# Kernel tuning notes

Measured on AMD Instinct MI355X. Metric: run time of the kernel, lower is better.

## Reference

```python
import jax, jax.numpy as jnp
import numpy as np


def _mlp(h, W1, b1, W2, b2):
    # Linear -> ReLU -> Linear
    h = jax.nn.relu(h @ W1 + b1)
    return h @ W2 + b2


def setup_inputs() -> dict:
    key = jax.random.key(0)
    ks = jax.random.split(key, 8)
    N, E, DN, DE, H, O = 50000, 800000, 128, 64, 256, 128
    DIN = DN + DE  # 192
    s1 = 1.0 / np.sqrt(DIN)
    s2 = 1.0 / np.sqrt(H)
    return {
        "x": jax.random.normal(ks[0], (N, DN), dtype=jnp.float32),
        "edge_index": jax.random.randint(ks[1], (2, E), 0, N, dtype=jnp.int32),
        "edge_attr": jax.random.normal(ks[2], (E, DE), dtype=jnp.float32),
        "W1_out": jax.random.normal(ks[3], (DIN, H), dtype=jnp.float32) * s1,
        "b1_out": jnp.zeros((H,), dtype=jnp.float32),
        "W2_out": jax.random.normal(ks[4], (H, O), dtype=jnp.float32) * s2,
        "b2_out": jnp.zeros((O,), dtype=jnp.float32),
        "W1_in": jax.random.normal(ks[5], (DIN, H), dtype=jnp.float32) * s1,
        "b1_in": jnp.zeros((H,), dtype=jnp.float32),
        "W2_in": jax.random.normal(ks[6], (H, O), dtype=jnp.float32) * s2,
        "b2_in": jnp.zeros((O,), dtype=jnp.float32),
    }


def reference(x, edge_index, edge_attr, W1_out, b1_out, W2_out, b2_out,
              W1_in, b1_in, W2_in, b2_in):
    N = x.shape[0]
    row, col = edge_index[0], edge_index[1]
    # Shared gather + concat: [E, d_node + d_edge]
    msg_in = jnp.concatenate([x[col], edge_attr], axis=1)

    # flow_out: edges with row < col. Compute MLP densely, zero masked edges,
    # then scatter-sum -> identical math to masked gather + scatter-sum.
    m_out = (row < col).astype(x.dtype)[:, None]
    flow_out = _mlp(msg_in, W1_out, b1_out, W2_out, b2_out) * m_out
    flow_out = jax.ops.segment_sum(flow_out, row, num_segments=N)

    # flow_in: edges with row > col
    m_in = (row > col).astype(x.dtype)[:, None]
    flow_in = _mlp(msg_in, W1_in, b1_in, W2_in, b2_in) * m_in
    flow_in = jax.ops.segment_sum(flow_in, row, num_segments=N)

    return jnp.concatenate((flow_in, flow_out), axis=1)  # [N, 2*O]
```

## Files before the change

kernel.cpp:

```cpp
#include <hip/hip_runtime.h>
#include <hip/hip_bf16.h>

typedef __attribute__((ext_vector_type(8))) short short8;
typedef __attribute__((ext_vector_type(8))) unsigned short ushort8;
typedef __attribute__((ext_vector_type(4))) float f32x4;

#define DN   128
#define DE   64
#define DIN  192
#define HID  256
#define OUTD 128
#define TE   128
#define NT   512
#define MSG_LD 200
#define H_LD   264
#define OUT_LD 132

static __device__ __forceinline__ unsigned short f2b(float f) {
    unsigned int u = __float_as_uint(f);
    u += 0x7fffu + ((u >> 16) & 1u);
    return (unsigned short)(u >> 16);
}

__global__ __launch_bounds__(256)
void prep_kernel(const float* __restrict__ W1o, const float* __restrict__ W1i,
                 const float* __restrict__ W2o, const float* __restrict__ W2i,
                 unsigned short* __restrict__ W1po, unsigned short* __restrict__ W1pi,
                 unsigned short* __restrict__ W2po, unsigned short* __restrict__ W2pi,
                 const int* __restrict__ ei, int E, int N, int* __restrict__ hist,
                 const float* __restrict__ x, unsigned short* __restrict__ xb) {
    const int S1 = DIN * HID, S2v = HID * OUTD;
    const int PACKN = 2 * S1 + 2 * S2v;
    int idx = blockIdx.x * blockDim.x + threadIdx.x;
    if (idx < PACKN) {
        const float* W; unsigned short* Wp; int Nc, j;
        if      (idx < S1)          { W = W1o; Wp = W1po; Nc = HID;  j = idx; }
        else if (idx < 2*S1)        { W = W1i; Wp = W1pi; Nc = HID;  j = idx - S1; }
        else if (idx < 2*S1 + S2v)  { W = W2o; Wp = W2po; Nc = OUTD; j = idx - 2*S1; }
        else                        { W = W2i; Wp = W2pi; Nc = OUTD; j = idx - 2*S1 - S2v; }
        int k = j / Nc, n = j - k * Nc;
        Wp[(((k >> 5) * Nc + n) << 5) + (k & 31)] = f2b(W[j]);
    } else if (idx < PACKN + E) {
        int e = idx - PACKN;
        int r = ei[e], c = ei[E + e];
        if      (r < c) atomicAdd(&hist[r], 1);
        else if (r > c) atomicAdd(&hist[N + r], 1);
    } else {
        int i = idx - PACKN - E;
        if (i < N * DN / 8) {
            float4 a = reinterpret_cast<const float4*>(x)[i * 2];
            float4 b = reinterpret_cast<const float4*>(x)[i * 2 + 1];
            ushort8 v = { f2b(a.x), f2b(a.y), f2b(a.z), f2b(a.w),
                          f2b(b.x), f2b(b.y), f2b(b.z), f2b(b.w) };
            reinterpret_cast<ushort8*>(xb)[i] = v;
        }
    }
}

__global__ __launch_bounds__(1024)
void scan1_kernel(const int* __restrict__ hist, int* __restrict__ cursor,
                  int* __restrict__ chunkSum, int N, int nch) {
    __shared__ int s_ws[16];
    const int br = blockIdx.x / nch, ch = blockIdx.x - br * nch;
    const int tid = threadIdx.x, lane = tid & 63, wv = tid >> 6;
    const int i = ch * 1024 + tid;
    int v = (i < N) ? hist[(size_t)br * N + i] : 0;
    int incl = v;
    #pragma unroll
    for (int d = 1; d < 64; d <<= 1) {
        int t = __shfl_up(incl, d, 64);
        if (lane >= d) incl += t;
    }
    if (lane == 63) s_ws[wv] = incl;
    __syncthreads();
    if (tid < 16) {
        int w = s_ws[tid];
        int wi = w;
        #pragma unroll
        for (int d = 1; d < 16; d <<= 1) {
            int t = __shfl_up(wi, d, 64);
            if (tid >= d) wi += t;
        }
        s_ws[tid] = wi - w;
    }
    __syncthreads();
    int excl = s_ws[wv] + incl - v;
    if (i < N) cursor[(size_t)br * N + i] = excl;
    if (tid == 1023) chunkSum[br * nch + ch] = excl + v;
}

__global__ __launch_bounds__(128)
void scan2_kernel(int* __restrict__ chunkSum, int* __restrict__ cnt, int nch) {
    const int br = threadIdx.x >> 6, lane = threadIdx.x & 63;
    int v = (lane < nch) ? chunkSum[br * nch + lane] : 0;
    int incl = v;
    #pragma unroll
    for (int d = 1; d < 64; d <<= 1) {
        int t = __shfl_up(incl, d, 64);
        if (lane >= d) incl += t;
    }
    if (lane < nch) chunkSum[br * nch + lane] = incl - v;
    if (lane == nch - 1) cnt[br] = incl;
}

__global__ __launch_bounds__(256)
void reorder_kernel(const int* __restrict__ ei, int E, int N, int nch,
                    int* __restrict__ cursor, const int* __restrict__ chunkSum,
                    int* __restrict__ list_out, int* __restrict__ list_in) {
    int e = blockIdx.x * blockDim.x + threadIdx.x;
    if (e >= E) return;
    int r = ei[e], c = ei[E + e];
    if (r == c) return;
    int br = (r < c) ? 0 : 1;
    int p = chunkSum[br * nch + (r >> 10)] + atomicAdd(&cursor[(size_t)br * N + r], 1);
    (br ? list_in : list_out)[p] = e;
}

__global__ __launch_bounds__(NT, 4)
void mlp_scatter_kernel(const unsigned short* __restrict__ xb,
                        const int* __restrict__ ei,
                        const float* __restrict__ ea,
                        const unsigned short* __restrict__ W1p_out,
                        const unsigned short* __restrict__ W1p_in,
                        const float* __restrict__ b1_out,
                        const float* __restrict__ b1_in,
                        const unsigned short* __restrict__ W2p_out,
                        const unsigned short* __restrict__ W2p_in,
                        const float* __restrict__ b2_out,
                        const float* __restrict__ b2_in,
                        const int* __restrict__ list_out,
                        const int* __restrict__ list_in,
                        const int* __restrict__ cnt,
                        float* __restrict__ out,
                        int E, int nbpb) {
    __shared__ __align__(16) unsigned short s_buf[TE * H_LD];
    __shared__ int s_eid[TE], s_dest[TE], s_col[TE];

    const int branch = (blockIdx.x >= nbpb) ? 1 : 0;
    const int lb = blockIdx.x - branch * nbpb;
    const int count = cnt[branch];
    if (lb * TE >= count) return;
    const int* list            = branch ? list_in : list_out;
    const unsigned short* W1p  = branch ? W1p_in  : W1p_out;
    const float* b1            = branch ? b1_in   : b1_out;
    const unsigned short* W2p  = branch ? W2p_in  : W2p_out;
    const float* b2            = branch ? b2_in   : b2_out;
    const int colbase          = branch ? 0 : OUTD;

    const int tid = threadIdx.x;
    if (tid < TE) {
        int idx = lb * TE + tid;
        int e = (idx < count) ? list[idx] : -1;
        s_eid[tid]  = e;
        s_dest[tid] = (e >= 0) ? ei[e] : -1;
        s_col[tid]  = (e >= 0) ? ei[E + e] : 0;
    }
    __syncthreads();

    {
        const int le  = tid >> 2;
        const int sub = tid & 3;
        const int e   = s_eid[le];
        const ushort8* xrow = reinterpret_cast<const ushort8*>(xb) + (size_t)s_col[le] * (DN / 8);
        #pragma unroll
        for (int j = 0; j < 4; ++j) {
            int seg = sub + j * 4;
            ushort8 v = {0, 0, 0, 0, 0, 0, 0, 0};
            if (e >= 0) v = xrow[seg];
            *reinterpret_cast<ushort8*>(&s_buf[le * MSG_LD + seg * 8]) = v;
        }
        const float4* erow = reinterpret_cast<const float4*>(ea) + (size_t)e * (DE / 4);
        #pragma unroll
        for (int j = 0; j < 4; ++j) {
            float4 v = make_float4(0.f, 0.f, 0.f, 0.f);
            if (e >= 0) v = erow[sub * 4 + j];
            unsigned int lo = (unsigned int)f2b(v.x) | ((unsigned int)f2b(v.y) << 16);
            unsigned int hi = (unsigned int)f2b(v.z) | ((unsigned int)f2b(v.w) << 16);
            *reinterpret_cast<uint2*>(&s_buf[le * MSG_LD + DN + sub * 16 + j * 4]) = make_uint2(lo, hi);
        }
    }
    __syncthreads();

    const int wave = tid >> 6;
    const int lane = tid & 63;
    const int ln   = lane & 15;
    const int quad = lane >> 4;

    f32x4 acc[8][2];
    {
        const int nbase = wave * 32;
        float bias[2];
        #pragma unroll
        for (int t = 0; t < 2; ++t) bias[t] = b1[nbase + t * 16 + ln];
        #pragma unroll
        for (int mt = 0; mt < 8; ++mt)
            #pragma unroll
            for (int t = 0; t < 2; ++t)
                acc[mt][t] = (f32x4){bias[t], bias[t], bias[t], bias[t]};
        #pragma unroll
        for (int kt = 0; kt < DIN / 32; ++kt) {
            short8 a[8], b[2];
            #pragma unroll
            for (int mt = 0; mt < 8; ++mt)
                a[mt] = *reinterpret_cast<const short8*>(
                    &s_buf[(mt * 16 + ln) * MSG_LD + kt * 32 + quad * 8]);
            #pragma unroll
            for (int t = 0; t < 2; ++t)
                b[t] = *reinterpret_cast<const short8*>(
                    &W1p[((kt * HID + nbase + t * 16 + ln) << 5) + quad * 8]);
            #pragma unroll
            for (int mt = 0; mt < 8; ++mt)
                #pragma unroll
                for (int t = 0; t < 2; ++t)
                    acc[mt][t] = __builtin_amdgcn_mfma_f32_16x16x32_bf16(a[mt], b[t], acc[mt][t], 0, 0, 0);
        }
    }
    __syncthreads();

    {
        const int nbase = wave * 32;
        #pragma unroll
        for (int mt = 0; mt < 8; ++mt)
            #pragma unroll
            for (int t = 0; t < 2; ++t) {
                int ncol = nbase + t * 16 + ln;
                #pragma unroll
                for (int r = 0; r < 4; ++r) {
                    int m = mt * 16 + quad * 4 + r;
                    float v = acc[mt][t][r];
                    s_buf[m * H_LD + ncol] = f2b(v > 0.f ? v : 0.f);
                }
            }
    }
    __syncthreads();

    f32x4 acc2[8];
    {
        const int nbase = wave * 16;
        float bias2 = b2[nbase + ln];
        #pragma unroll
        for (int mt = 0; mt < 8; ++mt)
            acc2[mt] = (f32x4){bias2, bias2, bias2, bias2};
        #pragma unroll
        for (int kt = 0; kt < HID / 32; ++kt) {
            short8 a[8], b;
            #pragma unroll
            for (int mt = 0; mt < 8; ++mt)
                a[mt] = *reinterpret_cast<const short8*>(
                    &s_buf[(mt * 16 + ln) * H_LD + kt * 32 + quad * 8]);
            b = *reinterpret_cast<const short8*>(
                &W2p[((kt * OUTD + nbase + ln) << 5) + quad * 8]);
            #pragma unroll
            for (int mt = 0; mt < 8; ++mt)
                acc2[mt] = __builtin_amdgcn_mfma_f32_16x16x32_bf16(a[mt], b, acc2[mt], 0, 0, 0);
        }
    }
    __syncthreads();

    float* s_outf = reinterpret_cast<float*>(s_buf);
    {
        const int nbase = wave * 16;
        #pragma unroll
        for (int mt = 0; mt < 8; ++mt)
            #pragma unroll
            for (int r = 0; r < 4; ++r)
                s_outf[(mt * 16 + quad * 4 + r) * OUT_LD + nbase + ln] = acc2[mt][r];
    }
    __syncthreads();

    {
        const int c  = tid & 127;
        const int m0 = (tid >> 7) * 32;
        float run = 0.f;
        int cur = -1, rs = m0;
        for (int m = m0; m < m0 + 32; ++m) {
            int d = s_dest[m];
            float v = s_outf[m * OUT_LD + c];
            if (d != cur) {
                if (cur >= 0) {
                    float* p = &out[(size_t)cur * (2 * OUTD) + colbase + c];
                    if (rs > m0) *p = run; else atomicAdd(p, run);
                }
                cur = d; run = 0.f; rs = m;
            }
            if (d >= 0) run += v;
        }
        if (cur >= 0)
            atomicAdd(&out[(size_t)cur * (2 * OUTD) + colbase + c], run);
    }
}

extern "C" void kernel_launch(void* const* d_in, const int* in_sizes, int n_in,
                              void* d_out, int out_size, void* d_ws, size_t ws_size,
                              hipStream_t stream) {
    const float* x   = (const float*)d_in[0];
    const int*   ei  = (const int*)d_in[1];
    const float* ea  = (const float*)d_in[2];
    const float* W1o = (const float*)d_in[3];
    const float* b1o = (const float*)d_in[4];
    const float* W2o = (const float*)d_in[5];
    const float* b2o = (const float*)d_in[6];
    const float* W1i = (const float*)d_in[7];
    const float* b1i = (const float*)d_in[8];
    const float* W2i = (const float*)d_in[9];
    const float* b2i = (const float*)d_in[10];
    float* out = (float*)d_out;
    const int E = in_sizes[1] / 2;
    const int N = in_sizes[0] / DN;
    const int nch = (N + 1023) >> 10;

    int* cnt      = (int*)d_ws;
    int* chunkSum = cnt + 16;
    int* hist     = chunkSum + 128;
    int* cursor   = hist + 2 * (size_t)N;
    int* list_out = cursor + 2 * (size_t)N;
    int* list_in  = list_out + E;
    unsigned short* W1po = (unsigned short*)(list_in + E);
    unsigned short* W1pi = W1po + DIN * HID;
    unsigned short* W2po = W1pi + DIN * HID;
    unsigned short* W2pi = W2po + HID * OUTD;
    unsigned short* xb   = W2pi + HID * OUTD;

    hipMemsetAsync(d_out, 0, (size_t)out_size * sizeof(float), stream);
    hipMemsetAsync(d_ws, 0, (576 + 8 * (size_t)N), stream);

    const int PACKN = 2 * DIN * HID + 2 * HID * OUTD;
    const int prepN = PACKN + E + N * DN / 8;
    prep_kernel<<<(prepN + 255) / 256, 256, 0, stream>>>(
        W1o, W1i, W2o, W2i, W1po, W1pi, W2po, W2pi, ei, E, N, hist, x, xb);

    scan1_kernel<<<2 * nch, 1024, 0, stream>>>(hist, cursor, chunkSum, N, nch);
    scan2_kernel<<<1, 128, 0, stream>>>(chunkSum, cnt, nch);
    reorder_kernel<<<(E + 255) / 256, 256, 0, stream>>>(
        ei, E, N, nch, cursor, chunkSum, list_out, list_in);

    const int nbpb = (E + TE - 1) / TE;
    mlp_scatter_kernel<<<2 * nbpb, NT, 0, stream>>>(
        xb, ei, ea, W1po, W1pi, b1o, b1i, W2po, W2pi, b2o, b2i,
        list_out, list_in, cnt, out, E, nbpb);
}
```

Baseline: 575.8 us.

## Shrink MLP tile to 64 edges, transpose-read hidden layer, pack launch grid

Halves the edge tile to 64 and the block to 256 threads. Each wave now computes a 4x4 tile of MFMA outputs in layer 1. The hidden activations are stored in a k-major packed layout and read back with ds_read_b64_tr_b16 transpose loads, with W2 fragments prefetched one step ahead. The grid is sized from the actual per-branch counts, so roughly half the blocks no longer launch only to exit, and bf16 conversion uses the hardware packed-convert instruction. The explicit waitcnt and sched_barrier pin the instruction order, and correctness depends on the inline-asm transpose layout matching the new store layout.

```diff
diff --git a/kernel.cpp b/kernel.cpp
--- a/kernel.cpp
+++ b/kernel.cpp
@@ -4,22 +4,38 @@
 typedef __attribute__((ext_vector_type(8))) short short8;
 typedef __attribute__((ext_vector_type(8))) unsigned short ushort8;
 typedef __attribute__((ext_vector_type(4))) float f32x4;
+typedef __attribute__((ext_vector_type(2))) unsigned int uint2v;
+typedef __attribute__((ext_vector_type(4))) unsigned int uint4v;
 
 #define DN   128
 #define DE   64
 #define DIN  192
 #define HID  256
 #define OUTD 128
-#define TE   128
-#define NT   512
+#define TE   64
+#define NT   256
 #define MSG_LD 200
-#define H_LD   264
 #define OUT_LD 132
+#define NMB  (TE / 16)
 
 static __device__ __forceinline__ unsigned short f2b(float f) {
     unsigned int u = __float_as_uint(f);
     u += 0x7fffu + ((u >> 16) & 1u);
     return (unsigned short)(u >> 16);
+}
+
+static __device__ __forceinline__ unsigned int cvt_pk2(float lo, float hi) {
+    unsigned int r;
+    asm("v_cvt_pk_bf16_f32 %0, %1, %2" : "=v"(r) : "v"(lo), "v"(hi));
+    return r;
+}
+
+template<int OFF>
+static __device__ __forceinline__ uint2v tr_read(unsigned addr) {
+    uint2v d;
+    asm volatile("ds_read_b64_tr_b16 %0, %1 offset:%c2"
+                 : "=v"(d) : "v"(addr), "n"(OFF));
+    return d;
 }
 
 __global__ __launch_bounds__(256)
@@ -132,13 +148,15 @@
                         const int* __restrict__ list_in,
                         const int* __restrict__ cnt,
                         float* __restrict__ out,
-                        int E, int nbpb) {
-    __shared__ __align__(16) unsigned short s_buf[TE * H_LD];
+                        int E) {
+    __shared__ __align__(16) unsigned short s_buf[TE * 264];
     __shared__ int s_eid[TE], s_dest[TE], s_col[TE];
 
-    const int branch = (blockIdx.x >= nbpb) ? 1 : 0;
-    const int lb = blockIdx.x - branch * nbpb;
-    const int count = cnt[branch];
+    const int c0 = cnt[0], c1 = cnt[1];
+    const int nb0 = (c0 + TE - 1) / TE;
+    const int branch = (blockIdx.x >= nb0) ? 1 : 0;
+    const int lb = branch ? (blockIdx.x - nb0) : blockIdx.x;
+    const int count = branch ? c1 : c0;
     if (lb * TE >= count) return;
     const int* list            = branch ? list_in : list_out;
     const unsigned short* W1p  = branch ? W1p_in  : W1p_out;
@@ -174,8 +192,8 @@
         for (int j = 0; j < 4; ++j) {
             float4 v = make_float4(0.f, 0.f, 0.f, 0.f);
             if (e >= 0) v = erow[sub * 4 + j];
-            unsigned int lo = (unsigned int)f2b(v.x) | ((unsigned int)f2b(v.y) << 16);
-            unsigned int hi = (unsigned int)f2b(v.z) | ((unsigned int)f2b(v.w) << 16);
+            unsigned int lo = cvt_pk2(v.x, v.y);
+            unsigned int hi = cvt_pk2(v.z, v.w);
             *reinterpret_cast<uint2*>(&s_buf[le * MSG_LD + DN + sub * 16 + j * 4]) = make_uint2(lo, hi);
         }
     }
@@ -186,85 +204,109 @@
     const int ln   = lane & 15;
     const int quad = lane >> 4;
 
-    f32x4 acc[8][2];
-    {
-        const int nbase = wave * 32;
-        float bias[2];
-        #pragma unroll
-        for (int t = 0; t < 2; ++t) bias[t] = b1[nbase + t * 16 + ln];
-        #pragma unroll
-        for (int mt = 0; mt < 8; ++mt)
-            #pragma unroll
-            for (int t = 0; t < 2; ++t)
+    f32x4 acc[4][4];
+    {
+        const int nbase = wave * 64;
+        float bias[4];
+        #pragma unroll
+        for (int t = 0; t < 4; ++t) bias[t] = b1[nbase + t * 16 + ln];
+        #pragma unroll
+        for (int mt = 0; mt < 4; ++mt)
+            #pragma unroll
+            for (int t = 0; t < 4; ++t)
                 acc[mt][t] = (f32x4){bias[t], bias[t], bias[t], bias[t]};
         #pragma unroll
         for (int kt = 0; kt < DIN / 32; ++kt) {
-            short8 a[8], b[2];
-            #pragma unroll
-            for (int mt = 0; mt < 8; ++mt)
+            short8 a[4], b[4];
+            #pragma unroll
+            for (int mt = 0; mt < 4; ++mt)
                 a[mt] = *reinterpret_cast<const short8*>(
                     &s_buf[(mt * 16 + ln) * MSG_LD + kt * 32 + quad * 8]);
             #pragma unroll
-            for (int t = 0; t < 2; ++t)
+            for (int t = 0; t < 4; ++t)
                 b[t] = *reinterpret_cast<const short8*>(
                     &W1p[((kt * HID + nbase + t * 16 + ln) << 5) + quad * 8]);
             #pragma unroll
-            for (int mt = 0; mt < 8; ++mt)
+            for (int mt = 0; mt < 4; ++mt)
                 #pragma unroll
-                for (int t = 0; t < 2; ++t)
+                for (int t = 0; t < 4; ++t)
                     acc[mt][t] = __builtin_amdgcn_mfma_f32_16x16x32_bf16(a[mt], b[t], acc[mt][t], 0, 0, 0);
         }
     }
     __syncthreads();
 
     {
-        const int nbase = wave * 32;
-        #pragma unroll
-        for (int mt = 0; mt < 8; ++mt)
-            #pragma unroll
-            for (int t = 0; t < 2; ++t) {
-                int ncol = nbase + t * 16 + ln;
+        const int nbase = wave * 64;
+        #pragma unroll
+        for (int mt = 0; mt < 4; ++mt)
+            #pragma unroll
+            for (int t = 0; t < 4; ++t) {
+                int n = nbase + t * 16 + ln;
+                float r0 = acc[mt][t][0], r1 = acc[mt][t][1];
+                float r2 = acc[mt][t][2], r3 = acc[mt][t][3];
+                r0 = r0 > 0.f ? r0 : 0.f;  r1 = r1 > 0.f ? r1 : 0.f;
+                r2 = r2 > 0.f ? r2 : 0.f;  r3 = r3 > 0.f ? r3 : 0.f;
+                unsigned int d0 = cvt_pk2(r0, r1);
+                unsigned int d1 = cvt_pk2(r2, r3);
+                int el = (((n >> 2) * NMB + mt) << 6) + ((n & 3) << 4) + (quad << 2);
+                *reinterpret_cast<uint2v*>(&s_buf[el]) = (uint2v){d0, d1};
+            }
+    }
+    __syncthreads();
+
+    f32x4 acc2[4][2];
+    {
+        const int nb2 = wave * 32;
+        float bz0 = b2[nb2 + ln];
+        float bz1 = b2[nb2 + 16 + ln];
+        #pragma unroll
+        for (int mt = 0; mt < 4; ++mt) {
+            acc2[mt][0] = (f32x4){bz0, bz0, bz0, bz0};
+            acc2[mt][1] = (f32x4){bz1, bz1, bz1, bz1};
+        }
+        const unsigned trb = (unsigned)(uintptr_t)(&s_buf[quad * 512 + ln * 4]);
+        short8 bn0 = *reinterpret_cast<const short8*>(&W2p[((nb2 + ln) << 5) + quad * 8]);
+        short8 bn1 = *reinterpret_cast<const short8*>(&W2p[((nb2 + 16 + ln) << 5) + quad * 8]);
+
+#define G2TR(kt, mt) { \
+        uint2v t0 = tr_read<(kt) * 4096 + (mt) * 128>(trb); \
+        uint2v t1 = tr_read<(kt) * 4096 + (mt) * 128 + 512>(trb); \
+        a[mt] = __builtin_bit_cast(short8, (uint4v){t0.x, t0.y, t1.x, t1.y}); }
+
+#define G2MM(mt) \
+        acc2[mt][0] = __builtin_amdgcn_mfma_f32_16x16x32_bf16(a[mt], b0c, acc2[mt][0], 0, 0, 0); \
+        acc2[mt][1] = __builtin_amdgcn_mfma_f32_16x16x32_bf16(a[mt], b1c, acc2[mt][1], 0, 0, 0);
+
+#define G2STEP(kt) { \
+        short8 a[4]; \
+        G2TR(kt, 0) G2TR(kt, 1) G2TR(kt, 2) G2TR(kt, 3) \
+        short8 b0c = bn0, b1c = bn1; \
+        if ((kt) < 7) { \
+            bn0 = *reinterpret_cast<const short8*>(&W2p[((((kt) + 1) * OUTD + nb2 + ln) << 5) + quad * 8]); \
+            bn1 = *reinterpret_cast<const short8*>(&W2p[((((kt) + 1) * OUTD + nb2 + 16 + ln) << 5) + quad * 8]); \
+        } \
+        asm volatile("s_waitcnt lgkmcnt(0)"); \
+        __builtin_amdgcn_sched_barrier(0); \
+        G2MM(0) G2MM(1) G2MM(2) G2MM(3) }
+
+        G2STEP(0) G2STEP(1) G2STEP(2) G2STEP(3)
+        G2STEP(4) G2STEP(5) G2STEP(6) G2STEP(7)
+#undef G2STEP
+#undef G2MM
+#undef G2TR
+    }
+    __syncthreads();
+
+    float* s_outf = reinterpret_cast<float*>(s_buf);
+    {
+        const int nb2 = wave * 32;
+        #pragma unroll
+        for (int mt = 0; mt < 4; ++mt)
+            #pragma unroll
+            for (int t = 0; t < 2; ++t)
                 #pragma unroll
-                for (int r = 0; r < 4; ++r) {
-                    int m = mt * 16 + quad * 4 + r;
-                    float v = acc[mt][t][r];
-                    s_buf[m * H_LD + ncol] = f2b(v > 0.f ? v : 0.f);
-                }
-            }
-    }
-    __syncthreads();
-
-    f32x4 acc2[8];
-    {
-        const int nbase = wave * 16;
-        float bias2 = b2[nbase + ln];
-        #pragma unroll
-        for (int mt = 0; mt < 8; ++mt)
-            acc2[mt] = (f32x4){bias2, bias2, bias2, bias2};
-        #pragma unroll
-        for (int kt = 0; kt < HID / 32; ++kt) {
-            short8 a[8], b;
-            #pragma unroll
-            for (int mt = 0; mt < 8; ++mt)
-                a[mt] = *reinterpret_cast<const short8*>(
-                    &s_buf[(mt * 16 + ln) * H_LD + kt * 32 + quad * 8]);
-            b = *reinterpret_cast<const short8*>(
-                &W2p[((kt * OUTD + nbase + ln) << 5) + quad * 8]);
-            #pragma unroll
-            for (int mt = 0; mt < 8; ++mt)
-                acc2[mt] = __builtin_amdgcn_mfma_f32_16x16x32_bf16(a[mt], b, acc2[mt], 0, 0, 0);
-        }
-    }
-    __syncthreads();
-
-    float* s_outf = reinterpret_cast<float*>(s_buf);
-    {
-        const int nbase = wave * 16;
-        #pragma unroll
-        for (int mt = 0; mt < 8; ++mt)
-            #pragma unroll
-            for (int r = 0; r < 4; ++r)
-                s_outf[(mt * 16 + quad * 4 + r) * OUT_LD + nbase + ln] = acc2[mt][r];
+                for (int r = 0; r < 4; ++r)
+                    s_outf[(mt * 16 + quad * 4 + r) * OUT_LD + nb2 + t * 16 + ln] = acc2[mt][t][r];
     }
     __syncthreads();
 
@@ -334,8 +376,8 @@
     reorder_kernel<<<(E + 255) / 256, 256, 0, stream>>>(
         ei, E, N, nch, cursor, chunkSum, list_out, list_in);
 
-    const int nbpb = (E + TE - 1) / TE;
-    mlp_scatter_kernel<<<2 * nbpb, NT, 0, stream>>>(
+    const int nblk = (E + TE - 1) / TE + 2;
+    mlp_scatter_kernel<<<nblk, NT, 0, stream>>>(
         xb, ei, ea, W1po, W1pi, b1o, b1i, W2po, W2pi, b2o, b2i,
-        list_out, list_in, cnt, out, E, nbpb);
-}
+        list_out, list_in, cnt, out, E);
+}
```

After: 573.7 us. About the same (-0.4%).
